# Performance work log

Measured on AMD Instinct MI355X. Metric: run time of the kernel, lower is better.

## Reference

```python
import jax, jax.numpy as jnp
import numpy as np

T, B, S, H, E, V = 16, 32, 256, 256, 300, 1000


def setup_inputs() -> dict:
    key = jax.random.key(0)
    ks = jax.random.split(key, 16)
    p = lambda k, shp: (jax.random.normal(k, shp, dtype=jnp.float32) * 0.05)
    return {
        "target_variable": jax.random.randint(ks[0], (T, B), 0, V),
        "h0": p(ks[1], (1, B, H)),
        "c0": p(ks[2], (1, B, H)),
        "encoder_outputs": jax.random.normal(ks[3], (S, B, H), dtype=jnp.float32),
        "encoder_lens": jax.random.randint(ks[4], (B,), 1, S + 1),
        "embedding": p(ks[5], (V, E)),
        "W_ih": p(ks[6], (4 * H, E)),
        "W_hh": p(ks[7], (4 * H, H)),
        "b_ih": p(ks[8], (4 * H,)),
        "b_hh": p(ks[9], (4 * H,)),
        "We": p(ks[10], (H, H)),
        "be": p(ks[11], (H,)),
        "Wd": p(ks[12], (H, H)),
        "bd": p(ks[13], (H,)),
        "wa": p(ks[14], (H,)),
        "ba": p(ks[14], (1,)),
        "W_out": p(ks[15], (V, 2 * H)),
        "b_out": p(ks[15], (V,)),
    }


def _lstm(x, h0, c0, W_ih, W_hh, b_ih, b_hh):
    # x: [T,B,E]; torch gate order i,f,g,o
    x_proj = jnp.einsum('tbe,ge->tbg', x, W_ih) + b_ih  # [T,B,4H]
    def step(carry, xg):
        h, c = carry
        g = xg + h @ W_hh.T + b_hh
        i, f, gg, o = jnp.split(g, 4, axis=-1)
        c = jax.nn.sigmoid(f) * c + jax.nn.sigmoid(i) * jnp.tanh(gg)
        h = jax.nn.sigmoid(o) * jnp.tanh(c)
        return (h, c), h
    (hT, cT), outs = jax.lax.scan(step, (h0[0], c0[0]), x_proj)
    return outs, hT[None], cT[None]


def reference(target_variable, h0, c0, encoder_outputs, encoder_lens,
              embedding, W_ih, W_hh, b_ih, b_hh,
              We, be, Wd, bd, wa, ba, W_out, b_out):
    emb = embedding[target_variable]                      # [T,B,E] (dropout p=0 -> identity)
    output, hT, cT = _lstm(emb, h0, c0, W_ih, W_hh, b_ih, b_hh)  # output [T,B,H]
    # additive attention: same math as expand+Linear, applied before broadcast
    enc_t = jnp.einsum('sbh,gh->sbg', encoder_outputs, We) + be   # [S,B,H]
    dec_t = jnp.einsum('tbh,gh->tbg', output, Wd) + bd            # [T,B,H]
    scores = jnp.einsum('tsbh,h->tsb', jnp.tanh(enc_t[None, :, :, :] + dec_t[:, None, :, :]), wa) + ba[0]
    raw_attention = jnp.transpose(scores, (2, 0, 1))              # [B,T,S]
    valid = (jnp.arange(S)[None, None, :] < encoder_lens[:, None, None])  # [B,1,S]
    raw_attention = jnp.where(valid, raw_attention, -jnp.inf)
    attention = jax.nn.softmax(raw_attention, axis=2)             # [B,T,S]
    enc_bf = jnp.transpose(encoder_outputs, (1, 0, 2))            # [B,S,H]
    context = jnp.einsum('bts,bsh->bth', attention, enc_bf)       # [B,T,H]
    out_bf = jnp.transpose(output, (1, 0, 2))                     # [B,T,H]
    combined = jnp.transpose(jnp.concatenate([context, out_bf], axis=2), (1, 0, 2))  # [T,B,2H]
    logits = jnp.einsum('tbh,vh->tbv', combined, W_out) + b_out
    output_prob = jax.nn.softmax(logits, axis=2)                  # [T,B,V]
    return output_prob, hT, cT, context
```

## Files before the change

kernel.cpp:

```cpp
#include <hip/hip_runtime.h>
#include <hip/hip_fp16.h>
#include <math.h>

typedef unsigned int u32;
typedef unsigned short u16;

#define T_ 16
#define B_ 32
#define S_ 256
#define H_ 256
#define E_ 300
#define V_ 1000

typedef _Float16 h2_t __attribute__((ext_vector_type(2)));
typedef __fp16  fp16v2 __attribute__((ext_vector_type(2)));

__device__ __forceinline__ float fast_tanh(float x) {
    return 1.0f - 2.0f / (__expf(2.0f * x) + 1.0f);
}
__device__ __forceinline__ float fast_sigm(float x) {
    return 1.0f / (1.0f + __expf(-x));
}
__device__ __forceinline__ float bf2f(u16 x) { return __uint_as_float(((u32)x) << 16); }
__device__ __forceinline__ float blo(u32 u) { return __uint_as_float(u << 16); }
__device__ __forceinline__ float bhi(u32 u) { return __uint_as_float(u & 0xffff0000u); }
__device__ __forceinline__ u16 f2bf(float f) {
    u32 u = __float_as_uint(f);
    u32 r = (u + 0x7fffu + ((u >> 16) & 1u)) >> 16;
    return (u16)r;
}
__device__ __forceinline__ h2_t u2h2(u32 u) {
    union { u32 a; h2_t b; } c; c.a = u; return c.b;
}
__device__ __forceinline__ u32 pk2(float a, float b) {
    union { fp16v2 v; u32 u; } c; c.v = __builtin_amdgcn_cvt_pkrtz(a, b); return c.u;
}
__device__ __forceinline__ float dot2f16(u32 w, u32 h, float acc) {
#if __has_builtin(__builtin_amdgcn_fdot2)
    return __builtin_amdgcn_fdot2(u2h2(w), u2h2(h), acc, false);
#else
    h2_t wv = u2h2(w), hv = u2h2(h);
    return acc + (float)wv.x * (float)hv.x + (float)wv.y * (float)hv.y;
#endif
}

__device__ void gemm_tile_256(const float* __restrict__ A, const int* __restrict__ gidx,
                              int lda, const float* __restrict__ Bw,
                              const float* __restrict__ bias, float* __restrict__ C,
                              int N, int K, int ldc, int bm, int bn)
{
    __shared__ float As[32][64];
    __shared__ float Bs[32][64];
    const int tid = threadIdx.x;
    const int ty = tid >> 4, tx = tid & 15;
    const int lr = tid >> 2;
    const int lk = (tid & 3) * 8;

    int am = bm + lr;
    int arow = gidx ? gidx[am] : am;
    const float* Ap = A + (size_t)arow * lda;
    int bnr = bn + lr;
    const float* Bp = (bnr < N) ? (Bw + (size_t)bnr * K) : nullptr;

    float acc[4][4] = {};

    for (int k0 = 0; k0 < K; k0 += 32) {
        int kb = k0 + lk;
        float av[8];
        if (kb + 8 <= K) {
            float4 p0 = *(const float4*)(Ap + kb);
            float4 p1 = *(const float4*)(Ap + kb + 4);
            av[0]=p0.x; av[1]=p0.y; av[2]=p0.z; av[3]=p0.w;
            av[4]=p1.x; av[5]=p1.y; av[6]=p1.z; av[7]=p1.w;
        } else {
            #pragma unroll
            for (int j = 0; j < 8; j++) av[j] = (kb + j < K) ? Ap[kb + j] : 0.0f;
        }
        #pragma unroll
        for (int j = 0; j < 8; j++) As[lk + j][lr] = av[j];
        if (Bp && kb + 8 <= K) {
            float4 p0 = *(const float4*)(Bp + kb);
            float4 p1 = *(const float4*)(Bp + kb + 4);
            av[0]=p0.x; av[1]=p0.y; av[2]=p0.z; av[3]=p0.w;
            av[4]=p1.x; av[5]=p1.y; av[6]=p1.z; av[7]=p1.w;
        } else if (Bp) {
            #pragma unroll
            for (int j = 0; j < 8; j++) av[j] = (kb + j < K) ? Bp[kb + j] : 0.0f;
        } else {
            #pragma unroll
            for (int j = 0; j < 8; j++) av[j] = 0.0f;
        }
        #pragma unroll
        for (int j = 0; j < 8; j++) Bs[lk + j][lr] = av[j];
        __syncthreads();
        #pragma unroll
        for (int kk = 0; kk < 32; kk++) {
            float4 a = *(const float4*)&As[kk][ty * 4];
            float4 b = *(const float4*)&Bs[kk][tx * 4];
            acc[0][0] += a.x*b.x; acc[0][1] += a.x*b.y; acc[0][2] += a.x*b.z; acc[0][3] += a.x*b.w;
            acc[1][0] += a.y*b.x; acc[1][1] += a.y*b.y; acc[1][2] += a.y*b.z; acc[1][3] += a.y*b.w;
            acc[2][0] += a.z*b.x; acc[2][1] += a.z*b.y; acc[2][2] += a.z*b.z; acc[2][3] += a.z*b.w;
            acc[3][0] += a.w*b.x; acc[3][1] += a.w*b.y; acc[3][2] += a.w*b.z; acc[3][3] += a.w*b.w;
        }
        __syncthreads();
    }
    #pragma unroll
    for (int i = 0; i < 4; i++) {
        int m = bm + ty * 4 + i;
        #pragma unroll
        for (int j = 0; j < 4; j++) {
            int n = bn + tx * 4 + j;
            if (n < N) C[(size_t)m * ldc + n] = acc[i][j] + bias[n];
        }
    }
}

__global__ __launch_bounds__(256)
void prep_xproj(const float* __restrict__ emb, const int* __restrict__ tv,
                const float* __restrict__ W_ih, const float* __restrict__ b_ih,
                float* __restrict__ xproj,
                const float* __restrict__ Whh,  u32* __restrict__ Wt2,
                const float* __restrict__ Wd,   float* __restrict__ Wdt,
                const float* __restrict__ W_out, u16* __restrict__ WoTb)
{
    const int bid = blockIdx.x;
    if (bid < 128) {
        gemm_tile_256(emb, tv, E_, W_ih, b_ih, xproj, 1024, E_, 1024,
                      (bid >> 4) * 64, (bid & 15) * 64);
        return;
    }
    __shared__ float tile[64][65];
    const int tid = threadIdx.x;
    const int wv = tid >> 6;
    const int lane = tid & 63;

    if (bid < 192) {
        int t = bid - 128;
        int r0 = (t >> 2) * 64, k0 = (t & 3) * 64;
        #pragma unroll 4
        for (int j = 0; j < 16; j++) {
            int row = wv * 16 + j;
            tile[row][lane] = Whh[(size_t)(r0 + row) * 256 + k0 + lane];
        }
        __syncthreads();
        #pragma unroll
        for (int it = 0; it < 2; it++) {
            int q = wv + 4 * it;
            uint4 val;
            val.x = pk2(tile[lane][8*q + 0], tile[lane][8*q + 1]);
            val.y = pk2(tile[lane][8*q + 2], tile[lane][8*q + 3]);
            val.z = pk2(tile[lane][8*q + 4], tile[lane][8*q + 5]);
            val.w = pk2(tile[lane][8*q + 6], tile[lane][8*q + 7]);
            ((uint4*)Wt2)[(size_t)((k0 >> 3) + q) * 1024 + r0 + lane] = val;
        }
    } else if (bid < 208) {
        int t = bid - 192;
        int h0 = (t >> 2) * 64, k0 = (t & 3) * 64;
        #pragma unroll 4
        for (int j = 0; j < 16; j++) {
            int row = wv * 16 + j;
            tile[row][lane] = Wd[(size_t)(h0 + row) * 256 + k0 + lane];
        }
        __syncthreads();
        #pragma unroll
        for (int it = 0; it < 4; it++) {
            int q = wv + 4 * it;
            float4 v;
            v.x = tile[lane][4*q + 0];
            v.y = tile[lane][4*q + 1];
            v.z = tile[lane][4*q + 2];
            v.w = tile[lane][4*q + 3];
            ((float4*)Wdt)[(size_t)((k0 >> 2) + q) * 256 + h0 + lane] = v;
        }
    } else {
        int t = bid - 208;
        int v0 = (t >> 3) * 64, k0 = (t & 7) * 64;
        #pragma unroll 4
        for (int j = 0; j < 16; j++) {
            int row = wv * 16 + j;
            int v = v0 + row;
            tile[row][lane] = (v < V_) ? W_out[(size_t)v * 512 + k0 + lane] : 0.0f;
        }
        __syncthreads();
        #pragma unroll
        for (int it = 0; it < 4; it++) {
            int q = wv + 4 * it;
            int v = v0 + lane;
            float a0 = tile[lane][4*q + 0], a1 = tile[lane][4*q + 1];
            float a2 = tile[lane][4*q + 2], a3 = tile[lane][4*q + 3];
            float b0 = __shfl_xor(a0, 1, 64), b1 = __shfl_xor(a1, 1, 64);
            float b2 = __shfl_xor(a2, 1, 64), b3 = __shfl_xor(a3, 1, 64);
            if (!(lane & 1) && v < V_) {
                uint4 w;
                w.x = (u32)f2bf(a0) | ((u32)f2bf(b0) << 16);
                w.y = (u32)f2bf(a1) | ((u32)f2bf(b1) << 16);
                w.z = (u32)f2bf(a2) | ((u32)f2bf(b2) << 16);
                w.w = (u32)f2bf(a3) | ((u32)f2bf(b3) << 16);
                ((uint4*)WoTb)[(size_t)((k0 >> 2) + q) * 500 + (v >> 1)] = w;
            }
        }
    }
}

__global__ __launch_bounds__(1024, 4)
void lstm_enct(const float* __restrict__ xproj,
               const u32*   __restrict__ Wt2,
               const float* __restrict__ bhh,
               const float* __restrict__ h0, const float* __restrict__ c0,
               float* __restrict__ combined,
               float* __restrict__ hT, float* __restrict__ cT,
               const float* __restrict__ enc_raw,
               const float* __restrict__ We,
               const float* __restrict__ be,
               float* __restrict__ enct)
{
    const int bid = blockIdx.x;
    const int tid = threadIdx.x;
    __shared__ __align__(16) u32 smem[38272];

    if (bid < 32) {
        float* zs = (float*)smem;
        float* cs = (float*)(smem + 1024);
        u32*   hp = smem + 1280;
        u32*   wlds = smem + 1408;
        float* hsave = (float*)(smem + 34176);
        const int b = bid;
        const int r = tid;
        if (tid < 256) {
            float h0v = h0[b * 256 + tid];
            cs[tid] = c0[b * 256 + tid];
            float hpart = __shfl_xor(h0v, 1, 64);
            if (!(tid & 1)) hp[tid >> 1] = pk2(h0v, hpart);
        }
        const float bh = bhh[r];
        const uint4* wp4 = (const uint4*)Wt2 + r;

        uint4 wreg[16];
        #pragma unroll
        for (int j = 0; j < 16; j++) wreg[j] = wp4[(size_t)(16 + j) * 1024];
        #pragma unroll
        for (int j = 0; j < 8; j++) {
            uint4 w = wp4[(size_t)(8 + j) * 1024];
            wlds[(j * 4 + 0) * 1024 + r] = w.x;
            wlds[(j * 4 + 1) * 1024 + r] = w.y;
            wlds[(j * 4 + 2) * 1024 + r] = w.z;
            wlds[(j * 4 + 3) * 1024 + r] = w.w;
        }
        __syncthreads();

        for (int t = 0; t < T_; t++) {
            float xp = xproj[((size_t)t * B_ + b) * 1024 + r];
            float acc = 0.0f;
            const uint4* hp4 = (const uint4*)hp;
            #pragma unroll
            for (int i = 0; i < 8; i++) {
                uint4 hv = hp4[i];
                uint4 w  = wp4[(size_t)i * 1024];
                acc = dot2f16(w.x, hv.x, acc);
                acc = dot2f16(w.y, hv.y, acc);
                acc = dot2f16(w.z, hv.z, acc);
                acc = dot2f16(w.w, hv.w, acc);
            }
            #pragma unroll
            for (int j = 0; j < 8; j++) {
                uint4 hv = hp4[8 + j];
                u32 w0 = wlds[(j * 4 + 0) * 1024 + r];
                u32 w1 = wlds[(j * 4 + 1) * 1024 + r];
                u32 w2 = wlds[(j * 4 + 2) * 1024 + r];
                u32 w3 = wlds[(j * 4 + 3) * 1024 + r];
                acc = dot2f16(w0, hv.x, acc);
                acc = dot2f16(w1, hv.y, acc);
                acc = dot2f16(w2, hv.z, acc);
                acc = dot2f16(w3, hv.w, acc);
            }
            #pragma unroll
            for (int j = 0; j < 16; j++) {
                uint4 hv = hp4[16 + j];
                acc = dot2f16(wreg[j].x, hv.x, acc);
                acc = dot2f16(wreg[j].y, hv.y, acc);
                acc = dot2f16(wreg[j].z, hv.z, acc);
                acc = dot2f16(wreg[j].w, hv.w, acc);
            }
            zs[r] = xp + bh + acc;
            __syncthreads();

            if (tid < 256) {
                float ig = fast_sigm(zs[tid]);
                float fg = fast_sigm(zs[256 + tid]);
                float gg = fast_tanh(zs[512 + tid]);
                float og = fast_sigm(zs[768 + tid]);
                float c = fg * cs[tid] + ig * gg;
                float h = og * fast_tanh(c);
                cs[tid] = c;
                hsave[(t << 8) + tid] = h;
                float hpart = __shfl_xor(h, 1, 64);
                if (!(tid & 1)) hp[tid >> 1] = pk2(h, hpart);
            }
            __syncthreads();
        }

        #pragma unroll
        for (int i = 0; i < 4; i++) {
            int idx = tid + i * 1024;
            int t = idx >> 8, h = idx & 255;
            combined[((size_t)t * B_ + b) * 512 + 256 + h] = hsave[idx];
        }
        if (tid < 256) {
            hT[b * 256 + tid] = hsave[(15 << 8) + tid];
            cT[b * 256 + tid] = cs[tid];
        }
    } else {
        float (*As2)[132] = (float (*)[132])smem;
        float (*Bs2)[132] = (float (*)[132])(smem + 4224);
        const int tile = bid - 32;
        const int bm = (tile >> 1) * 128;
        const int bn = (tile & 1) * 128;
        const int tx = tid & 31, ty = tid >> 5;
        const int lr = tid >> 3;
        const int lk = (tid & 7) * 4;

        const float* Ap = enc_raw + (size_t)(bm + lr) * 256;
        const float* Bp = We + (size_t)(bn + lr) * 256;
        float acc[4][4] = {};

        for (int k0 = 0; k0 < 256; k0 += 32) {
            float4 a4 = *(const float4*)(Ap + k0 + lk);
            float4 b4 = *(const float4*)(Bp + k0 + lk);
            As2[lk + 0][lr] = a4.x; As2[lk + 1][lr] = a4.y;
            As2[lk + 2][lr] = a4.z; As2[lk + 3][lr] = a4.w;
            Bs2[lk + 0][lr] = b4.x; Bs2[lk + 1][lr] = b4.y;
            Bs2[lk + 2][lr] = b4.z; Bs2[lk + 3][lr] = b4.w;
            __syncthreads();
            #pragma unroll
            for (int kk = 0; kk < 32; kk++) {
                float4 a = *(const float4*)&As2[kk][ty * 4];
                float4 b = *(const float4*)&Bs2[kk][tx * 4];
                acc[0][0] += a.x*b.x; acc[0][1] += a.x*b.y; acc[0][2] += a.x*b.z; acc[0][3] += a.x*b.w;
                acc[1][0] += a.y*b.x; acc[1][1] += a.y*b.y; acc[1][2] += a.y*b.z; acc[1][3] += a.y*b.w;
                acc[2][0] += a.z*b.x; acc[2][1] += a.z*b.y; acc[2][2] += a.z*b.z; acc[2][3] += a.z*b.w;
                acc[3][0] += a.w*b.x; acc[3][1] += a.w*b.y; acc[3][2] += a.w*b.z; acc[3][3] += a.w*b.w;
            }
            __syncthreads();
        }
        #pragma unroll
        for (int i = 0; i < 4; i++) {
            int m = bm + ty * 4 + i;
            #pragma unroll
            for (int j = 0; j < 4; j++) {
                int n = bn + tx * 4 + j;
                enct[(size_t)m * 256 + n] = acc[i][j] + be[n];
            }
        }
    }
}

__global__ __launch_bounds__(512)
void attn_logits(const float* __restrict__ enct,
                 const float* __restrict__ combined_in,
                 const float* __restrict__ Wdt,
                 const float* __restrict__ bd,
                 const float* __restrict__ enc_raw,
                 const float* __restrict__ wa, const float* __restrict__ ba,
                 const int* __restrict__ lens,
                 const u16* __restrict__ WoTb,
                 const float* __restrict__ b_out,
                 float* __restrict__ ctx_out,
                 float* __restrict__ probs)
{
    const int bid = blockIdx.x;
    const int b = bid & 31;
    const int t = bid >> 5;
    const int tid = threadIdx.x;
    const int wv = tid >> 6, lane = tid & 63;
    __shared__ float ds[256], was[256], sc[256];
    __shared__ float crow[512];
    __shared__ float tmp2[512];
    __shared__ float lrow[1000];
    __shared__ float red[8], red2[8];

    if (tid < 256) {
        crow[256 + tid] = combined_in[((size_t)t * B_ + b) * 512 + 256 + tid];
        was[tid] = wa[tid];
    }
    const int len = lens[b];
    const float bav = ba[0];
    __syncthreads();

    {
        const int h   = tid & 255;
        const int kq0 = (tid >> 8) * 32;
        float acc = 0.0f;
        const float4* wp = (const float4*)Wdt + h;
        #pragma unroll 8
        for (int kq = kq0; kq < kq0 + 32; kq++) {
            float4 w = wp[(size_t)kq * 256];
            float4 c = *(const float4*)&crow[256 + kq * 4];
            acc += w.x * c.x;
            acc += w.y * c.y;
            acc += w.z * c.z;
            acc += w.w * c.w;
        }
        tmp2[tid] = acc;
    }
    __syncthreads();
    if (tid < 256) ds[tid] = bd[tid] + tmp2[tid] + tmp2[tid + 256];
    __syncthreads();

    for (int s = wv; s < len; s += 8) {
        const float* er = enct + ((size_t)s * B_ + b) * 256;
        float sum = 0.0f;
        #pragma unroll
        for (int j = 0; j < 4; j++) {
            int h = lane + 64 * j;
            sum += fast_tanh(er[h] + ds[h]) * was[h];
        }
        #pragma unroll
        for (int off = 32; off >= 1; off >>= 1) sum += __shfl_xor(sum, off, 64);
        if (lane == 0) sc[s] = sum + bav;
    }
    __syncthreads();

    float x = (tid < len) ? sc[tid] : -INFINITY;
    float m = x;
    #pragma unroll
    for (int off = 32; off >= 1; off >>= 1) m = fmaxf(m, __shfl_xor(m, off, 64));
    if (lane == 0) red[wv] = m;
    __syncthreads();
    m = red[0];
    #pragma unroll
    for (int i = 1; i < 8; i++) m = fmaxf(m, red[i]);
    float e = __expf(x - m);
    float ssum = e;
    #pragma unroll
    for (int off = 32; off >= 1; off >>= 1) ssum += __shfl_xor(ssum, off, 64);
    if (lane == 0) red2[wv] = ssum;
    __syncthreads();
    ssum = red2[0] + red2[1] + red2[2] + red2[3] + red2[4] + red2[5] + red2[6] + red2[7];
    if (tid < 256) sc[tid] = e / ssum;
    __syncthreads();

    {
        const int h  = tid & 255;
        const int sg = tid >> 8;
        const int mid = (len + 1) >> 1;
        const int s0 = sg ? mid : 0;
        const int s1 = sg ? len : mid;
        float cacc = 0.0f;
        const float* eb = enc_raw + (size_t)b * 256 + h;
        #pragma unroll 4
        for (int s = s0; s < s1; s++) cacc += sc[s] * eb[(size_t)s * (B_ * H_)];
        tmp2[tid] = cacc;
    }
    __syncthreads();
    if (tid < 256) {
        float ctx = tmp2[tid] + tmp2[tid + 256];
        ctx_out[((size_t)b * T_ + t) * 256 + tid] = ctx;
        crow[tid] = ctx;
    }
    __syncthreads();

    if (tid < 500) {
        const int v0 = tid * 2;
        float a0 = b_out[v0], a1 = b_out[v0 + 1];
        const uint4* wp = (const uint4*)WoTb + tid;
        #pragma unroll 8
        for (int kq = 0; kq < 128; kq++) {
            uint4 w = wp[(size_t)kq * 500];
            float4 c = *(const float4*)&crow[kq * 4];
            a0 += c.x * blo(w.x); a1 += c.x * bhi(w.x);
            a0 += c.y * blo(w.y); a1 += c.y * bhi(w.y);
            a0 += c.z * blo(w.z); a1 += c.z * bhi(w.z);
            a0 += c.w * blo(w.w); a1 += c.w * bhi(w.w);
        }
        lrow[v0] = a0;
        lrow[v0 + 1] = a1;
    }
    __syncthreads();

    float v0v = -INFINITY, v1v = -INFINITY;
    if (tid < 500) { v0v = lrow[tid * 2]; v1v = lrow[tid * 2 + 1]; }
    float mx = fmaxf(v0v, v1v);
    #pragma unroll
    for (int off = 32; off >= 1; off >>= 1) mx = fmaxf(mx, __shfl_xor(mx, off, 64));
    if (lane == 0) red[wv] = mx;
    __syncthreads();
    mx = red[0];
    #pragma unroll
    for (int i = 1; i < 8; i++) mx = fmaxf(mx, red[i]);
    float e0 = __expf(v0v - mx), e1 = __expf(v1v - mx);
    float s2 = e0 + e1;
    #pragma unroll
    for (int off = 32; off >= 1; off >>= 1) s2 += __shfl_xor(s2, off, 64);
    if (lane == 0) red2[wv] = s2;
    __syncthreads();
    s2 = red2[0] + red2[1] + red2[2] + red2[3] + red2[4] + red2[5] + red2[6] + red2[7];
    float inv = 1.0f / s2;
    if (tid < 500) {
        float2 pv = make_float2(e0 * inv, e1 * inv);
        *(float2*)&probs[((size_t)t * B_ + b) * V_ + tid * 2] = pv;
    }
}

extern "C" void kernel_launch(void* const* d_in, const int* in_sizes, int n_in,
                              void* d_out, int out_size, void* d_ws, size_t ws_size,
                              hipStream_t stream) {
    const int*   tv       = (const int*)d_in[0];
    const float* h0       = (const float*)d_in[1];
    const float* c0       = (const float*)d_in[2];
    const float* enc_raw  = (const float*)d_in[3];
    const int*   lens     = (const int*)d_in[4];
    const float* emb      = (const float*)d_in[5];
    const float* W_ih     = (const float*)d_in[6];
    const float* W_hh     = (const float*)d_in[7];
    const float* b_ih     = (const float*)d_in[8];
    const float* b_hh     = (const float*)d_in[9];
    const float* We       = (const float*)d_in[10];
    const float* be       = (const float*)d_in[11];
    const float* Wd       = (const float*)d_in[12];
    const float* bd       = (const float*)d_in[13];
    const float* wa       = (const float*)d_in[14];
    const float* ba       = (const float*)d_in[15];
    const float* W_out    = (const float*)d_in[16];
    const float* b_out    = (const float*)d_in[17];

    float* ws       = (float*)d_ws;
    float* enct     = ws;
    float* xproj    = ws + 2097152;
    float* Wdt      = ws + 2621440;
    u16*   WoTb     = (u16*)(ws + 2752512);
    float* combined = ws + 3264512;
    u32*   Wt2      = (u32*)(ws + 3526656);

    float* out      = (float*)d_out;
    float* probs    = out;
    float* hT       = out + 512000;
    float* cT       = out + 520192;
    float* ctx_out  = out + 528384;

    prep_xproj<<<336, 256, 0, stream>>>(emb, tv, W_ih, b_ih, xproj,
                                        W_hh, Wt2, Wd, Wdt, W_out, WoTb);
    lstm_enct<<<160, 1024, 0, stream>>>(xproj, Wt2, b_hh, h0, c0, combined, hT, cT,
                                        enc_raw, We, be, enct);
    attn_logits<<<512, 512, 0, stream>>>(enct, combined, Wdt, bd, enc_raw,
                                         wa, ba, lens, WoTb, b_out, ctx_out, probs);
}
```

Baseline: 217.6 us.

## Move Wd/W_out transposes into LSTM kernel and shrink x-projection tiles

Moves the Wd and W_out transpose/convert blocks out of the prep kernel and into the LSTM/enc-projection kernel as extra blocks, so they run alongside the serial LSTM recurrence rather than ahead of it. Replaces the 64x64 x-projection GEMM tile with 32x64 tiles, giving twice as many blocks for the embedding-input projection to shorten the prep critical path. The LSTM kernel's occupancy hint changes from a launch_bounds min-blocks argument to an explicit waves-per-EU attribute. The cost is a larger grid for the LSTM kernel, whose extra blocks may compete for CUs with the recurrence blocks.

Result: faster. 208.7 us (-4.1%).

```diff
diff --git a/kernel.cpp b/kernel.cpp
--- a/kernel.cpp
+++ b/kernel.cpp
@@ -44,165 +44,103 @@
 #endif
 }
 
-__device__ void gemm_tile_256(const float* __restrict__ A, const int* __restrict__ gidx,
-                              int lda, const float* __restrict__ Bw,
-                              const float* __restrict__ bias, float* __restrict__ C,
-                              int N, int K, int ldc, int bm, int bn)
-{
-    __shared__ float As[32][64];
-    __shared__ float Bs[32][64];
-    const int tid = threadIdx.x;
-    const int ty = tid >> 4, tx = tid & 15;
-    const int lr = tid >> 2;
-    const int lk = (tid & 3) * 8;
-
-    int am = bm + lr;
-    int arow = gidx ? gidx[am] : am;
-    const float* Ap = A + (size_t)arow * lda;
-    int bnr = bn + lr;
-    const float* Bp = (bnr < N) ? (Bw + (size_t)bnr * K) : nullptr;
-
-    float acc[4][4] = {};
-
-    for (int k0 = 0; k0 < K; k0 += 32) {
-        int kb = k0 + lk;
-        float av[8];
-        if (kb + 8 <= K) {
-            float4 p0 = *(const float4*)(Ap + kb);
-            float4 p1 = *(const float4*)(Ap + kb + 4);
-            av[0]=p0.x; av[1]=p0.y; av[2]=p0.z; av[3]=p0.w;
-            av[4]=p1.x; av[5]=p1.y; av[6]=p1.z; av[7]=p1.w;
-        } else {
-            #pragma unroll
-            for (int j = 0; j < 8; j++) av[j] = (kb + j < K) ? Ap[kb + j] : 0.0f;
-        }
-        #pragma unroll
-        for (int j = 0; j < 8; j++) As[lk + j][lr] = av[j];
-        if (Bp && kb + 8 <= K) {
-            float4 p0 = *(const float4*)(Bp + kb);
-            float4 p1 = *(const float4*)(Bp + kb + 4);
-            av[0]=p0.x; av[1]=p0.y; av[2]=p0.z; av[3]=p0.w;
-            av[4]=p1.x; av[5]=p1.y; av[6]=p1.z; av[7]=p1.w;
-        } else if (Bp) {
-            #pragma unroll
-            for (int j = 0; j < 8; j++) av[j] = (kb + j < K) ? Bp[kb + j] : 0.0f;
-        } else {
-            #pragma unroll
-            for (int j = 0; j < 8; j++) av[j] = 0.0f;
-        }
-        #pragma unroll
-        for (int j = 0; j < 8; j++) Bs[lk + j][lr] = av[j];
-        __syncthreads();
-        #pragma unroll
-        for (int kk = 0; kk < 32; kk++) {
-            float4 a = *(const float4*)&As[kk][ty * 4];
-            float4 b = *(const float4*)&Bs[kk][tx * 4];
-            acc[0][0] += a.x*b.x; acc[0][1] += a.x*b.y; acc[0][2] += a.x*b.z; acc[0][3] += a.x*b.w;
-            acc[1][0] += a.y*b.x; acc[1][1] += a.y*b.y; acc[1][2] += a.y*b.z; acc[1][3] += a.y*b.w;
-            acc[2][0] += a.z*b.x; acc[2][1] += a.z*b.y; acc[2][2] += a.z*b.z; acc[2][3] += a.z*b.w;
-            acc[3][0] += a.w*b.x; acc[3][1] += a.w*b.y; acc[3][2] += a.w*b.z; acc[3][3] += a.w*b.w;
-        }
-        __syncthreads();
-    }
-    #pragma unroll
-    for (int i = 0; i < 4; i++) {
-        int m = bm + ty * 4 + i;
-        #pragma unroll
-        for (int j = 0; j < 4; j++) {
-            int n = bn + tx * 4 + j;
-            if (n < N) C[(size_t)m * ldc + n] = acc[i][j] + bias[n];
-        }
-    }
-}
-
 __global__ __launch_bounds__(256)
 void prep_xproj(const float* __restrict__ emb, const int* __restrict__ tv,
                 const float* __restrict__ W_ih, const float* __restrict__ b_ih,
                 float* __restrict__ xproj,
-                const float* __restrict__ Whh,  u32* __restrict__ Wt2,
-                const float* __restrict__ Wd,   float* __restrict__ Wdt,
-                const float* __restrict__ W_out, u16* __restrict__ WoTb)
+                const float* __restrict__ Whh,  u32* __restrict__ Wt2)
 {
     const int bid = blockIdx.x;
-    if (bid < 128) {
-        gemm_tile_256(emb, tv, E_, W_ih, b_ih, xproj, 1024, E_, 1024,
-                      (bid >> 4) * 64, (bid & 15) * 64);
+    const int tid = threadIdx.x;
+    if (bid < 256) {
+        __shared__ float As[32][33];
+        __shared__ float Bs[32][64];
+        const int bm = (bid >> 4) * 32;
+        const int bn = (bid & 15) * 64;
+        const int ty = tid >> 4;
+        const int tx = tid & 15;
+        const int alr = tid >> 3;
+        const int alk = (tid & 7) * 4;
+        const int blr = tid >> 2;
+        const int blk = (tid & 3) * 8;
+
+        const float* Ap = emb + (size_t)tv[bm + alr] * E_;
+        const float* Bp = W_ih + (size_t)(bn + blr) * E_;
+
+        float acc[2][4] = {};
+        for (int k0 = 0; k0 < E_; k0 += 32) {
+            int kb = k0 + alk;
+            float4 a4;
+            if (kb + 4 <= E_) {
+                a4 = *(const float4*)(Ap + kb);
+            } else {
+                a4.x = (kb + 0 < E_) ? Ap[kb + 0] : 0.0f;
+                a4.y = (kb + 1 < E_) ? Ap[kb + 1] : 0.0f;
+                a4.z = (kb + 2 < E_) ? Ap[kb + 2] : 0.0f;
+                a4.w = (kb + 3 < E_) ? Ap[kb + 3] : 0.0f;
+            }
+            As[alk + 0][alr] = a4.x; As[alk + 1][alr] = a4.y;
+            As[alk + 2][alr] = a4.z; As[alk + 3][alr] = a4.w;
+
+            int kbb = k0 + blk;
+            float bv[8];
+            if (kbb + 8 <= E_) {
+                float4 p0 = *(const float4*)(Bp + kbb);
+                float4 p1 = *(const float4*)(Bp + kbb + 4);
+                bv[0]=p0.x; bv[1]=p0.y; bv[2]=p0.z; bv[3]=p0.w;
+                bv[4]=p1.x; bv[5]=p1.y; bv[6]=p1.z; bv[7]=p1.w;
+            } else {
+                #pragma unroll
+                for (int j = 0; j < 8; j++) bv[j] = (kbb + j < E_) ? Bp[kbb + j] : 0.0f;
+            }
+            #pragma unroll
+            for (int j = 0; j < 8; j++) Bs[blk + j][blr] = bv[j];
+            __syncthreads();
+            #pragma unroll
+            for (int kk = 0; kk < 32; kk++) {
+                float ax = As[kk][ty * 2], ay = As[kk][ty * 2 + 1];
+                float4 b = *(const float4*)&Bs[kk][tx * 4];
+                acc[0][0] += ax*b.x; acc[0][1] += ax*b.y; acc[0][2] += ax*b.z; acc[0][3] += ax*b.w;
+                acc[1][0] += ay*b.x; acc[1][1] += ay*b.y; acc[1][2] += ay*b.z; acc[1][3] += ay*b.w;
+            }
+            __syncthreads();
+        }
+        #pragma unroll
+        for (int i = 0; i < 2; i++) {
+            int m = bm + ty * 2 + i;
+            #pragma unroll
+            for (int j = 0; j < 4; j++) {
+                int n = bn + tx * 4 + j;
+                xproj[(size_t)m * 1024 + n] = acc[i][j] + b_ih[n];
+            }
+        }
         return;
     }
     __shared__ float tile[64][65];
-    const int tid = threadIdx.x;
     const int wv = tid >> 6;
     const int lane = tid & 63;
-
-    if (bid < 192) {
-        int t = bid - 128;
-        int r0 = (t >> 2) * 64, k0 = (t & 3) * 64;
-        #pragma unroll 4
-        for (int j = 0; j < 16; j++) {
-            int row = wv * 16 + j;
-            tile[row][lane] = Whh[(size_t)(r0 + row) * 256 + k0 + lane];
-        }
-        __syncthreads();
-        #pragma unroll
-        for (int it = 0; it < 2; it++) {
-            int q = wv + 4 * it;
-            uint4 val;
-            val.x = pk2(tile[lane][8*q + 0], tile[lane][8*q + 1]);
-            val.y = pk2(tile[lane][8*q + 2], tile[lane][8*q + 3]);
-            val.z = pk2(tile[lane][8*q + 4], tile[lane][8*q + 5]);
-            val.w = pk2(tile[lane][8*q + 6], tile[lane][8*q + 7]);
-            ((uint4*)Wt2)[(size_t)((k0 >> 3) + q) * 1024 + r0 + lane] = val;
-        }
-    } else if (bid < 208) {
-        int t = bid - 192;
-        int h0 = (t >> 2) * 64, k0 = (t & 3) * 64;
-        #pragma unroll 4
-        for (int j = 0; j < 16; j++) {
-            int row = wv * 16 + j;
-            tile[row][lane] = Wd[(size_t)(h0 + row) * 256 + k0 + lane];
-        }
-        __syncthreads();
-        #pragma unroll
-        for (int it = 0; it < 4; it++) {
-            int q = wv + 4 * it;
-            float4 v;
-            v.x = tile[lane][4*q + 0];
-            v.y = tile[lane][4*q + 1];
-            v.z = tile[lane][4*q + 2];
-            v.w = tile[lane][4*q + 3];
-            ((float4*)Wdt)[(size_t)((k0 >> 2) + q) * 256 + h0 + lane] = v;
-        }
-    } else {
-        int t = bid - 208;
-        int v0 = (t >> 3) * 64, k0 = (t & 7) * 64;
-        #pragma unroll 4
-        for (int j = 0; j < 16; j++) {
-            int row = wv * 16 + j;
-            int v = v0 + row;
-            tile[row][lane] = (v < V_) ? W_out[(size_t)v * 512 + k0 + lane] : 0.0f;
-        }
-        __syncthreads();
-        #pragma unroll
-        for (int it = 0; it < 4; it++) {
-            int q = wv + 4 * it;
-            int v = v0 + lane;
-            float a0 = tile[lane][4*q + 0], a1 = tile[lane][4*q + 1];
-            float a2 = tile[lane][4*q + 2], a3 = tile[lane][4*q + 3];
-            float b0 = __shfl_xor(a0, 1, 64), b1 = __shfl_xor(a1, 1, 64);
-            float b2 = __shfl_xor(a2, 1, 64), b3 = __shfl_xor(a3, 1, 64);
-            if (!(lane & 1) && v < V_) {
-                uint4 w;
-                w.x = (u32)f2bf(a0) | ((u32)f2bf(b0) << 16);
-                w.y = (u32)f2bf(a1) | ((u32)f2bf(b1) << 16);
-                w.z = (u32)f2bf(a2) | ((u32)f2bf(b2) << 16);
-                w.w = (u32)f2bf(a3) | ((u32)f2bf(b3) << 16);
-                ((uint4*)WoTb)[(size_t)((k0 >> 2) + q) * 500 + (v >> 1)] = w;
-            }
-        }
-    }
-}
-
-__global__ __launch_bounds__(1024, 4)
+    int t = bid - 256;
+    int r0 = (t >> 2) * 64, k0 = (t & 3) * 64;
+    #pragma unroll 4
+    for (int j = 0; j < 16; j++) {
+        int row = wv * 16 + j;
+        tile[row][lane] = Whh[(size_t)(r0 + row) * 256 + k0 + lane];
+    }
+    __syncthreads();
+    #pragma unroll
+    for (int it = 0; it < 2; it++) {
+        int q = wv + 4 * it;
+        uint4 val;
+        val.x = pk2(tile[lane][8*q + 0], tile[lane][8*q + 1]);
+        val.y = pk2(tile[lane][8*q + 2], tile[lane][8*q + 3]);
+        val.z = pk2(tile[lane][8*q + 4], tile[lane][8*q + 5]);
+        val.w = pk2(tile[lane][8*q + 6], tile[lane][8*q + 7]);
+        ((uint4*)Wt2)[(size_t)((k0 >> 3) + q) * 1024 + r0 + lane] = val;
+    }
+}
+
+__global__ __launch_bounds__(1024)
+__attribute__((amdgpu_waves_per_eu(4, 4)))
 void lstm_enct(const float* __restrict__ xproj,
                const u32*   __restrict__ Wt2,
                const float* __restrict__ bhh,
@@ -212,7 +150,9 @@
                const float* __restrict__ enc_raw,
                const float* __restrict__ We,
                const float* __restrict__ be,
-               float* __restrict__ enct)
+               float* __restrict__ enct,
+               const float* __restrict__ Wd,   float* __restrict__ Wdt,
+               const float* __restrict__ W_out, u16* __restrict__ WoTb)
 {
     const int bid = blockIdx.x;
     const int tid = threadIdx.x;
@@ -309,7 +249,7 @@
             hT[b * 256 + tid] = hsave[(15 << 8) + tid];
             cT[b * 256 + tid] = cs[tid];
         }
-    } else {
+    } else if (bid < 160) {
         float (*As2)[132] = (float (*)[132])smem;
         float (*Bs2)[132] = (float (*)[132])(smem + 4224);
         const int tile = bid - 32;
@@ -349,6 +289,56 @@
             for (int j = 0; j < 4; j++) {
                 int n = bn + tx * 4 + j;
                 enct[(size_t)m * 256 + n] = acc[i][j] + be[n];
+            }
+        }
+    } else if (bid < 176) {
+        float (*tile)[65] = (float (*)[65])smem;
+        const int w = tid >> 6;
+        const int lane = tid & 63;
+        int t = bid - 160;
+        int h0 = (t >> 2) * 64, k0 = (t & 3) * 64;
+        #pragma unroll
+        for (int j = 0; j < 4; j++) {
+            int row = w * 4 + j;
+            tile[row][lane] = Wd[(size_t)(h0 + row) * 256 + k0 + lane];
+        }
+        __syncthreads();
+        {
+            int q = w;
+            float4 v;
+            v.x = tile[lane][4*q + 0];
+            v.y = tile[lane][4*q + 1];
+            v.z = tile[lane][4*q + 2];
+            v.w = tile[lane][4*q + 3];
+            ((float4*)Wdt)[(size_t)((k0 >> 2) + q) * 256 + h0 + lane] = v;
+        }
+    } else {
+        float (*tile)[65] = (float (*)[65])smem;
+        const int w = tid >> 6;
+        const int lane = tid & 63;
+        int t = bid - 176;
+        int v0 = (t >> 3) * 64, k0 = (t & 7) * 64;
+        #pragma unroll
+        for (int j = 0; j < 4; j++) {
+            int row = w * 4 + j;
+            int v = v0 + row;
+            tile[row][lane] = (v < V_) ? W_out[(size_t)v * 512 + k0 + lane] : 0.0f;
+        }
+        __syncthreads();
+        {
+            int q = w;
+            int v = v0 + lane;
+            float a0 = tile[lane][4*q + 0], a1 = tile[lane][4*q + 1];
+            float a2 = tile[lane][4*q + 2], a3 = tile[lane][4*q + 3];
+            float b0 = __shfl_xor(a0, 1, 64), b1 = __shfl_xor(a1, 1, 64);
+            float b2 = __shfl_xor(a2, 1, 64), b3 = __shfl_xor(a3, 1, 64);
+            if (!(lane & 1) && v < V_) {
+                uint4 wq;
+                wq.x = (u32)f2bf(a0) | ((u32)f2bf(b0) << 16);
+                wq.y = (u32)f2bf(a1) | ((u32)f2bf(b1) << 16);
+                wq.z = (u32)f2bf(a2) | ((u32)f2bf(b2) << 16);
+                wq.w = (u32)f2bf(a3) | ((u32)f2bf(b3) << 16);
+                ((uint4*)WoTb)[(size_t)((k0 >> 2) + q) * 500 + (v >> 1)] = wq;
             }
         }
     }
@@ -537,10 +527,10 @@
     float* cT       = out + 520192;
     float* ctx_out  = out + 528384;
 
-    prep_xproj<<<336, 256, 0, stream>>>(emb, tv, W_ih, b_ih, xproj,
-                                        W_hh, Wt2, Wd, Wdt, W_out, WoTb);
-    lstm_enct<<<160, 1024, 0, stream>>>(xproj, Wt2, b_hh, h0, c0, combined, hT, cT,
-                                        enc_raw, We, be, enct);
+    prep_xproj<<<320, 256, 0, stream>>>(emb, tv, W_ih, b_ih, xproj, W_hh, Wt2);
+    lstm_enct<<<304, 1024, 0, stream>>>(xproj, Wt2, b_hh, h0, c0, combined, hT, cT,
+                                        enc_raw, We, be, enct,
+                                        Wd, Wdt, W_out, WoTb);
     attn_logits<<<512, 512, 0, stream>>>(enct, combined, Wdt, bd, enc_raw,
                                          wa, ba, lens, WoTb, b_out, ctx_out, probs);
 }
```
